# Kernel optimization log

Hardware: AMD Instinct MI355X
Metric: run time of the kernel (lower is better)

Reference implementation:

```python
import jax, jax.numpy as jnp
import numpy as np

PAD = 0

def setup_inputs() -> dict:
    key = jax.random.key(0)
    k1, k2, k3, k4 = jax.random.split(key, 4)
    B, S, F, V, H, D = 64, 256, 4, 50257, 768, 512
    words = jax.random.randint(k1, (B, S, F), 0, V, dtype=jnp.int64)  # pad_index=0 occurs rarely at random
    E = jax.random.normal(k2, (V, H), dtype=jnp.float32) * 0.02      # stand-in for transformer last_hidden_state producer
    W = jax.random.normal(k3, (H, D), dtype=jnp.float32) * 0.02      # FFN projection weight
    b = jax.random.normal(k4, (D,), dtype=jnp.float32) * 0.02
    return {"words": words, "E": E, "W": W, "b": b}

def reference(words, E, W, b):
    # words: [B, S, F] subword ids; mask out pad subwords
    mask = (words != PAD)                                  # [B,S,F] bool
    sub = E[words] * mask[..., None].astype(E.dtype)       # [B,S,F,H], pads zeroed
    cnt = mask.sum(-1).astype(E.dtype)                     # [B,S] subwords per word
    # segment-mean over the fix_len axis; fully-padded words -> 0 (matches pad_sequence(..., 0))
    word_emb = sub.sum(-2) / jnp.maximum(cnt, 1.0)[..., None]   # [B,S,H]
    word_emb = jnp.where((cnt > 0)[..., None], word_emb, 0.0)
    return word_emb @ W + b                                # [B,S,D]
```

## Files before the change

### kernel.cpp

```cpp
#include <hip/hip_runtime.h>
#include <hip/hip_bf16.h>

#define M_TOT 16384
#define K_TOT 768
#define N_TOT 512
#define NT 12

typedef __attribute__((ext_vector_type(8))) __bf16 bf16x8;
typedef __attribute__((ext_vector_type(4))) float f32x4;

static __device__ __forceinline__ ushort f2bf(float x) {
  union { float f; unsigned int u; } v; v.f = x;
  unsigned int r = v.u + 0x7fffu + ((v.u >> 16) & 1u);
  return (ushort)(r >> 16);
}
static __device__ __forceinline__ unsigned pack2(float lo, float hi) {
  return (unsigned)f2bf(lo) | ((unsigned)f2bf(hi) << 16);
}

__global__ __launch_bounds__(256) void wt_kernel(const float* __restrict__ W,
                                                 ushort* __restrict__ Wt) {
  __shared__ float tile[64][65];
  const int t  = threadIdx.x;
  const int k0 = blockIdx.x * 64;
  const int n0 = blockIdx.y * 64;
#pragma unroll
  for (int i = 0; i < 4; ++i) {
    const int idx = t + i * 256;
    const int r = idx >> 4;
    const int c = (idx & 15) * 4;
    const float4 v =
        *reinterpret_cast<const float4*>(W + (size_t)(k0 + r) * N_TOT + n0 + c);
    tile[r][c + 0] = v.x; tile[r][c + 1] = v.y;
    tile[r][c + 2] = v.z; tile[r][c + 3] = v.w;
  }
  __syncthreads();
#pragma unroll
  for (int i = 0; i < 4; ++i) {
    const int idx = t + i * 256;
    const int rn = idx >> 4;
    const int ck = (idx & 15) * 4;
    ushort4 o;
    o.x = f2bf(tile[ck + 0][rn]);
    o.y = f2bf(tile[ck + 1][rn]);
    o.z = f2bf(tile[ck + 2][rn]);
    o.w = f2bf(tile[ck + 3][rn]);
    const int kg    = k0 + ck;
    const int chunk = kg >> 3;
    const int e0    = kg & 7;
    *reinterpret_cast<ushort4*>(
        &Wt[((size_t)chunk * N_TOT + n0 + rn) * 8 + e0]) = o;
  }
}

__global__ __launch_bounds__(512, 1) void fused_kernel(
    const int* __restrict__ words, const float* __restrict__ E,
    const ushort* __restrict__ Wt, const float* __restrict__ bias,
    float* __restrict__ out) {
  __shared__ ushort A0[32 * 96 * 8];
  __shared__ ushort A1[32 * 96 * 8];
  __shared__ int   eoff_l[64][4];
  __shared__ float msk_l[64][4];
  __shared__ float scl_l[64];

  const int t    = threadIdx.x;
  const int lane = t & 63;
  const int w    = t >> 6;
  const int bm   = blockIdx.x;
  const int w4   = w * 4;

  if (t < 64) {
    const int4 wd =
        *reinterpret_cast<const int4*>(words + (size_t)(bm * 64 + t) * 4);
    const int ids[4] = {wd.x, wd.y, wd.z, wd.w};
    float cnt = 0.f;
#pragma unroll
    for (int f = 0; f < 4; ++f) {
      eoff_l[t][f] = ids[f] * K_TOT;
      const float m = (ids[f] != 0) ? 1.f : 0.f;
      msk_l[t][f] = m;
      cnt += m;
    }
    scl_l[t] = (cnt > 0.f) ? (1.f / cnt) : 0.f;
  }
  __syncthreads();

  float4 vA[12], vB[12];

#define G_LOAD(vv, grow)                                                     \
  do {                                                                       \
    const int row_ = (grow);                                                 \
    _Pragma("unroll") for (int f = 0; f < 4; ++f) {                          \
      const float4* p_ =                                                     \
          reinterpret_cast<const float4*>(E + eoff_l[row_][f]) + lane;       \
      vv[f * 3 + 0] = p_[0];                                                 \
      vv[f * 3 + 1] = p_[64];                                                \
      vv[f * 3 + 2] = p_[128];                                               \
    }                                                                        \
  } while (0)

#define G_MATH(vv, grow, dstA, lrow)                                         \
  do {                                                                       \
    const int row_ = (grow);                                                 \
    const float km0 = msk_l[row_][0], km1 = msk_l[row_][1];                  \
    const float km2 = msk_l[row_][2], km3 = msk_l[row_][3];                  \
    const float ksc = scl_l[row_];                                           \
    _Pragma("unroll") for (int c = 0; c < 3; ++c) {                          \
      float s[4];                                                            \
      _Pragma("unroll") for (int j = 0; j < 4; ++j)                          \
        s[j] = (vv[0 * 3 + c][j] * km0 + vv[1 * 3 + c][j] * km1 +            \
                vv[2 * 3 + c][j] * km2 + vv[3 * 3 + c][j] * km3) * ksc;      \
      uint2 o_;                                                              \
      o_.x = pack2(s[0], s[1]);                                              \
      o_.y = pack2(s[2], s[3]);                                              \
      const int slot_ = c * 32 + ((lane >> 1) ^ (row_ & 7));                 \
      *reinterpret_cast<uint2*>(                                             \
          &(dstA)[(lrow) * 768 + slot_ * 8 + (lane & 1) * 4]) = o_;          \
    }                                                                        \
  } while (0)

  const int rsel = lane & 15;
  const int ksel = lane >> 4;
  const int colBase = w * 64 + rsel;
  f32x4 acc[2][4];

#define COMPUTE(Asrc, kt)                                                    \
  do {                                                                       \
    _Pragma("unroll") for (int kk = 0; kk < 2; ++kk) {                       \
      const int g = (kt) * 8 + kk * 4 + ksel;                                \
      bf16x8 af[2], bfr[4];                                                  \
      _Pragma("unroll") for (int m = 0; m < 2; ++m) {                        \
        const int r_ = m * 16 + rsel;                                        \
        af[m] = *reinterpret_cast<const bf16x8*>(                            \
            &(Asrc)[r_ * 768 + ((g ^ (r_ & 7))) * 8]);                       \
      }                                                                      \
      _Pragma("unroll") for (int n = 0; n < 4; ++n)                          \
        bfr[n] = *reinterpret_cast<const bf16x8*>(                           \
            &Wt[((size_t)g * N_TOT + colBase + n * 16) * 8]);                \
      __builtin_amdgcn_s_setprio(1);                                         \
      _Pragma("unroll") for (int m = 0; m < 2; ++m)                          \
        _Pragma("unroll") for (int n = 0; n < 4; ++n)                        \
          acc[m][n] = __builtin_amdgcn_mfma_f32_16x16x32_bf16(               \
              af[m], bfr[n], acc[m][n], 0, 0, 0);                            \
      __builtin_amdgcn_s_setprio(0);                                         \
    }                                                                        \
  } while (0)

#define EPILOGUE(T)                                                          \
  do {                                                                       \
    const int row0 = bm * 64 + (T) * 32 + (ksel << 2);                       \
    _Pragma("unroll") for (int n = 0; n < 4; ++n) {                          \
      const float bv = bias[colBase + n * 16];                               \
      _Pragma("unroll") for (int m = 0; m < 2; ++m) {                        \
        _Pragma("unroll") for (int j = 0; j < 4; ++j) {                      \
          __builtin_nontemporal_store(                                       \
              acc[m][n][j] + bv,                                             \
              &out[(size_t)(row0 + m * 16 + j) * N_TOT + colBase + n * 16]); \
        }                                                                    \
      }                                                                      \
    }                                                                        \
  } while (0)

  G_LOAD(vA, w4 + 0);
  G_LOAD(vB, w4 + 1);
  G_MATH(vA, w4 + 0, A0, w4 + 0);  G_LOAD(vA, w4 + 2);
  G_MATH(vB, w4 + 1, A0, w4 + 1);  G_LOAD(vB, w4 + 3);
  G_MATH(vA, w4 + 2, A0, w4 + 2);
  G_MATH(vB, w4 + 3, A0, w4 + 3);
  __syncthreads();

#pragma unroll
  for (int m = 0; m < 2; ++m)
#pragma unroll
    for (int n = 0; n < 4; ++n) acc[m][n] = (f32x4){0.f, 0.f, 0.f, 0.f};

  __builtin_amdgcn_sched_barrier(0);
  G_LOAD(vA, 32 + w4 + 0);
  G_LOAD(vB, 32 + w4 + 1);
  __builtin_amdgcn_sched_barrier(0);
  COMPUTE(A0, 0);  COMPUTE(A0, 1);  COMPUTE(A0, 2);
  COMPUTE(A0, 3);  COMPUTE(A0, 4);  COMPUTE(A0, 5);
  G_MATH(vA, 32 + w4 + 0, A1, w4 + 0);
  G_MATH(vB, 32 + w4 + 1, A1, w4 + 1);
  __builtin_amdgcn_sched_barrier(0);
  G_LOAD(vA, 32 + w4 + 2);
  G_LOAD(vB, 32 + w4 + 3);
  __builtin_amdgcn_sched_barrier(0);
  COMPUTE(A0, 6);  COMPUTE(A0, 7);  COMPUTE(A0, 8);
  COMPUTE(A0, 9);  COMPUTE(A0, 10); COMPUTE(A0, 11);
  G_MATH(vA, 32 + w4 + 2, A1, w4 + 2);
  G_MATH(vB, 32 + w4 + 3, A1, w4 + 3);
  EPILOGUE(0);
  __syncthreads();

#pragma unroll
  for (int m = 0; m < 2; ++m)
#pragma unroll
    for (int n = 0; n < 4; ++n) acc[m][n] = (f32x4){0.f, 0.f, 0.f, 0.f};
#pragma unroll
  for (int kt = 0; kt < NT; ++kt) COMPUTE(A1, kt);
  EPILOGUE(1);

#undef G_LOAD
#undef G_MATH
#undef COMPUTE
#undef EPILOGUE
}

extern "C" void kernel_launch(void* const* d_in, const int* in_sizes, int n_in,
                              void* d_out, int out_size, void* d_ws,
                              size_t ws_size, hipStream_t stream) {
  const int*   words = (const int*)d_in[0];
  const float* E     = (const float*)d_in[1];
  const float* W     = (const float*)d_in[2];
  const float* b     = (const float*)d_in[3];
  float* out = (float*)d_out;

  ushort* Wtws = (ushort*)d_ws;

  hipLaunchKernelGGL(wt_kernel, dim3(K_TOT / 64, N_TOT / 64), dim3(256), 0,
                     stream, W, Wtws);
  hipLaunchKernelGGL(fused_kernel, dim3(M_TOT / 64), dim3(512), 0, stream,
                     words, E, Wtws, b, out);
}
```

Before: 56.81 us.

## Split fused kernel into producer gather waves and consumer MFMA waves

Launches 768 threads per block. Eight waves gather, mask and average embedding rows into two LDS buffers, and four other waves run the bf16 MFMA GEMM over 128 output columns each. This replaces the previous interleaved schedule in which every wave both gathered and computed. The aim is to overlap the gather with the matrix math through wave specialization. In exchange, consumer register pressure is higher, fewer waves issue MFMA, and the design depends on barriers matching across divergent branches.

```diff
diff --git a/kernel.cpp b/kernel.cpp
--- a/kernel.cpp
+++ b/kernel.cpp
@@ -53,7 +53,7 @@
   }
 }
 
-__global__ __launch_bounds__(512, 1) void fused_kernel(
+__global__ __launch_bounds__(768, 1) void fused_kernel(
     const int* __restrict__ words, const float* __restrict__ E,
     const ushort* __restrict__ Wt, const float* __restrict__ bias,
     float* __restrict__ out) {
@@ -67,7 +67,6 @@
   const int lane = t & 63;
   const int w    = t >> 6;
   const int bm   = blockIdx.x;
-  const int w4   = w * 4;
 
   if (t < 64) {
     const int4 wd =
@@ -85,11 +84,13 @@
   }
   __syncthreads();
 
-  float4 vA[12], vB[12];
-
-#define G_LOAD(vv, grow)                                                     \
-  do {                                                                       \
-    const int row_ = (grow);                                                 \
+  if (w < 8) {
+    const int p4 = w * 4;
+    float4 vA[12], vB[12];
+
+#define G_LOAD(vv, S, r)                                                     \
+  do {                                                                       \
+    const int row_ = (S) * 32 + p4 + (r);                                    \
     _Pragma("unroll") for (int f = 0; f < 4; ++f) {                          \
       const float4* p_ =                                                     \
           reinterpret_cast<const float4*>(E + eoff_l[row_][f]) + lane;       \
@@ -99,9 +100,10 @@
     }                                                                        \
   } while (0)
 
-#define G_MATH(vv, grow, dstA, lrow)                                         \
-  do {                                                                       \
-    const int row_ = (grow);                                                 \
+#define G_MATH(vv, S, r, dstA)                                               \
+  do {                                                                       \
+    const int row_ = (S) * 32 + p4 + (r);                                    \
+    const int lrow_ = p4 + (r);                                              \
     const float km0 = msk_l[row_][0], km1 = msk_l[row_][1];                  \
     const float km2 = msk_l[row_][2], km3 = msk_l[row_][3];                  \
     const float ksc = scl_l[row_];                                           \
@@ -113,43 +115,60 @@
       uint2 o_;                                                              \
       o_.x = pack2(s[0], s[1]);                                              \
       o_.y = pack2(s[2], s[3]);                                              \
-      const int slot_ = c * 32 + ((lane >> 1) ^ (row_ & 7));                 \
+      const int slot_ = c * 32 + ((lane >> 1) ^ (lrow_ & 7));                \
       *reinterpret_cast<uint2*>(                                             \
-          &(dstA)[(lrow) * 768 + slot_ * 8 + (lane & 1) * 4]) = o_;          \
-    }                                                                        \
-  } while (0)
-
-  const int rsel = lane & 15;
-  const int ksel = lane >> 4;
-  const int colBase = w * 64 + rsel;
-  f32x4 acc[2][4];
-
-#define COMPUTE(Asrc, kt)                                                    \
+          &(dstA)[lrow_ * 768 + slot_ * 8 + (lane & 1) * 4]) = o_;           \
+    }                                                                        \
+  } while (0)
+
+    G_LOAD(vA, 0, 0);       G_LOAD(vB, 0, 1);
+    G_MATH(vA, 0, 0, A0);   G_LOAD(vA, 0, 2);
+    G_MATH(vB, 0, 1, A0);   G_LOAD(vB, 0, 3);
+    G_MATH(vA, 0, 2, A0);
+    G_MATH(vB, 0, 3, A0);
+    __syncthreads();
+
+    G_LOAD(vA, 1, 0);       G_LOAD(vB, 1, 1);
+    G_MATH(vA, 1, 0, A1);   G_LOAD(vA, 1, 2);
+    G_MATH(vB, 1, 1, A1);   G_LOAD(vB, 1, 3);
+    G_MATH(vA, 1, 2, A1);
+    G_MATH(vB, 1, 3, A1);
+    __syncthreads();
+#undef G_LOAD
+#undef G_MATH
+  } else {
+    const int cw   = w - 8;
+    const int rsel = lane & 15;
+    const int ksel = lane >> 4;
+    const int colBase = cw * 128 + rsel;
+    f32x4 acc[2][8];
+
+#define C_COMPUTE(Asrc, kt)                                                  \
   do {                                                                       \
     _Pragma("unroll") for (int kk = 0; kk < 2; ++kk) {                       \
       const int g = (kt) * 8 + kk * 4 + ksel;                                \
-      bf16x8 af[2], bfr[4];                                                  \
+      bf16x8 af[2], bfr[8];                                                  \
       _Pragma("unroll") for (int m = 0; m < 2; ++m) {                        \
         const int r_ = m * 16 + rsel;                                        \
         af[m] = *reinterpret_cast<const bf16x8*>(                            \
             &(Asrc)[r_ * 768 + ((g ^ (r_ & 7))) * 8]);                       \
       }                                                                      \
-      _Pragma("unroll") for (int n = 0; n < 4; ++n)                          \
+      _Pragma("unroll") for (int n = 0; n < 8; ++n)                          \
         bfr[n] = *reinterpret_cast<const bf16x8*>(                           \
             &Wt[((size_t)g * N_TOT + colBase + n * 16) * 8]);                \
       __builtin_amdgcn_s_setprio(1);                                         \
       _Pragma("unroll") for (int m = 0; m < 2; ++m)                          \
-        _Pragma("unroll") for (int n = 0; n < 4; ++n)                        \
+        _Pragma("unroll") for (int n = 0; n < 8; ++n)                        \
           acc[m][n] = __builtin_amdgcn_mfma_f32_16x16x32_bf16(               \
               af[m], bfr[n], acc[m][n], 0, 0, 0);                            \
       __builtin_amdgcn_s_setprio(0);                                         \
     }                                                                        \
   } while (0)
 
-#define EPILOGUE(T)                                                          \
-  do {                                                                       \
-    const int row0 = bm * 64 + (T) * 32 + (ksel << 2);                       \
-    _Pragma("unroll") for (int n = 0; n < 4; ++n) {                          \
+#define C_EPILOGUE(S)                                                        \
+  do {                                                                       \
+    const int row0 = bm * 64 + (S) * 32 + (ksel << 2);                       \
+    _Pragma("unroll") for (int n = 0; n < 8; ++n) {                          \
       const float bv = bias[colBase + n * 16];                               \
       _Pragma("unroll") for (int m = 0; m < 2; ++m) {                        \
         _Pragma("unroll") for (int j = 0; j < 4; ++j) {                      \
@@ -161,50 +180,25 @@
     }                                                                        \
   } while (0)
 
-  G_LOAD(vA, w4 + 0);
-  G_LOAD(vB, w4 + 1);
-  G_MATH(vA, w4 + 0, A0, w4 + 0);  G_LOAD(vA, w4 + 2);
-  G_MATH(vB, w4 + 1, A0, w4 + 1);  G_LOAD(vB, w4 + 3);
-  G_MATH(vA, w4 + 2, A0, w4 + 2);
-  G_MATH(vB, w4 + 3, A0, w4 + 3);
-  __syncthreads();
-
-#pragma unroll
-  for (int m = 0; m < 2; ++m)
-#pragma unroll
-    for (int n = 0; n < 4; ++n) acc[m][n] = (f32x4){0.f, 0.f, 0.f, 0.f};
-
-  __builtin_amdgcn_sched_barrier(0);
-  G_LOAD(vA, 32 + w4 + 0);
-  G_LOAD(vB, 32 + w4 + 1);
-  __builtin_amdgcn_sched_barrier(0);
-  COMPUTE(A0, 0);  COMPUTE(A0, 1);  COMPUTE(A0, 2);
-  COMPUTE(A0, 3);  COMPUTE(A0, 4);  COMPUTE(A0, 5);
-  G_MATH(vA, 32 + w4 + 0, A1, w4 + 0);
-  G_MATH(vB, 32 + w4 + 1, A1, w4 + 1);
-  __builtin_amdgcn_sched_barrier(0);
-  G_LOAD(vA, 32 + w4 + 2);
-  G_LOAD(vB, 32 + w4 + 3);
-  __builtin_amdgcn_sched_barrier(0);
-  COMPUTE(A0, 6);  COMPUTE(A0, 7);  COMPUTE(A0, 8);
-  COMPUTE(A0, 9);  COMPUTE(A0, 10); COMPUTE(A0, 11);
-  G_MATH(vA, 32 + w4 + 2, A1, w4 + 2);
-  G_MATH(vB, 32 + w4 + 3, A1, w4 + 3);
-  EPILOGUE(0);
-  __syncthreads();
-
-#pragma unroll
-  for (int m = 0; m < 2; ++m)
-#pragma unroll
-    for (int n = 0; n < 4; ++n) acc[m][n] = (f32x4){0.f, 0.f, 0.f, 0.f};
-#pragma unroll
-  for (int kt = 0; kt < NT; ++kt) COMPUTE(A1, kt);
-  EPILOGUE(1);
-
-#undef G_LOAD
-#undef G_MATH
-#undef COMPUTE
-#undef EPILOGUE
+    __syncthreads();
+#pragma unroll
+    for (int m = 0; m < 2; ++m)
+#pragma unroll
+      for (int n = 0; n < 8; ++n) acc[m][n] = (f32x4){0.f, 0.f, 0.f, 0.f};
+#pragma unroll
+    for (int kt = 0; kt < NT; ++kt) C_COMPUTE(A0, kt);
+    C_EPILOGUE(0);
+    __syncthreads();
+#pragma unroll
+    for (int m = 0; m < 2; ++m)
+#pragma unroll
+      for (int n = 0; n < 8; ++n) acc[m][n] = (f32x4){0.f, 0.f, 0.f, 0.f};
+#pragma unroll
+    for (int kt = 0; kt < NT; ++kt) C_COMPUTE(A1, kt);
+    C_EPILOGUE(1);
+#undef C_COMPUTE
+#undef C_EPILOGUE
+  }
 }
 
 extern "C" void kernel_launch(void* const* d_in, const int* in_sizes, int n_in,
@@ -220,6 +214,6 @@
 
   hipLaunchKernelGGL(wt_kernel, dim3(K_TOT / 64, N_TOT / 64), dim3(256), 0,
                      stream, W, Wtws);
-  hipLaunchKernelGGL(fused_kernel, dim3(M_TOT / 64), dim3(512), 0, stream,
+  hipLaunchKernelGGL(fused_kernel, dim3(M_TOT / 64), dim3(768), 0, stream,
                      words, E, Wtws, b, out);
 }
```

Result: slower. 117.9 us (+107.5%).
